# Kernel optimization log

Hardware: AMD Instinct MI355X
Metric: run time of the kernel (lower is better)

Reference implementation:

```python
import jax, jax.numpy as jnp
import numpy as np

N_ITER = 5
NMF_EPS = 1e-20
IP_EPS = 1e-20

M, J, I, K = 2, 2000, 2049, 8  # channels == sources, frames, freq bins, NMF bases


def setup_inputs() -> dict:
    key = jax.random.key(0)
    k1, k2, k3 = jax.random.split(key, 3)
    X = jax.random.normal(k1, (M, J, I, 2), dtype=jnp.float32)
    lo = 1e-08
    T0 = jax.random.uniform(k2, (I, K, M), dtype=jnp.float32) * (1 - lo) + lo
    V0 = jax.random.uniform(k3, (K, J, M), dtype=jnp.float32) * (1 - lo) + lo
    return {"X": X, "T0": T0, "V0": V0}


def nmf_update(T, V, Y, eps):
    # T: (I,K), V: (K,J), Y: (I,J) complex
    P = jnp.abs(Y) ** 2                       # power spectrogram (I,J)
    R = T @ V                                  # low-rank model (I,J)
    T = T * jnp.sqrt(((P / (R * R)) @ V.T) / ((1.0 / R) @ V.T))
    T = jnp.maximum(T, eps)
    R = T @ V
    V = V * jnp.sqrt((T.T @ (P / (R * R))) / (T.T @ (1.0 / R)))
    V = jnp.maximum(V, eps)
    R = T @ V
    return T, V, R


def reference(X, T0, V0):
    Mc, Jc, Ic, _ = X.shape
    N = Mc
    # view_as_complex(X.permute(2,0,1,3)) -> (I, M, J) complex
    Xc = jnp.transpose(X[..., 0] + 1j * X[..., 1], (2, 0, 1)).astype(jnp.complex64)
    eye_M = jnp.eye(Mc, dtype=jnp.complex64)
    W = jnp.broadcast_to(eye_M, (Ic, N, Mc))   # (I, N, M)
    T, V = T0, V0

    def body(carry, _):
        W, T, V = carry
        Y = jnp.einsum('inm,imj->inj', W, Xc)  # (I, N, J)
        for n in range(N):
            Tn, Vn, Rn = nmf_update(T[:, :, n], V[:, :, n], Y[:, n, :], NMF_EPS)
            T = T.at[:, :, n].set(Tn)
            V = V.at[:, :, n].set(Vn)
            inv_Rn = 1.0 / (Rn + IP_EPS)                       # (I, J)
            Xw = Xc * jnp.sqrt(inv_Rn)[:, None, :]             # (I, M, J)
            D = jnp.einsum('imj,ikj->imk', Xw, jnp.conj(Xw)) / Jc  # (I, M, M)
            Dreg = D + IP_EPS * eye_M
            A = jnp.einsum('inm,imk->ink', W, Dreg)            # (I, M, M)
            e_n = jnp.broadcast_to(eye_M[:, n], (Ic, Mc))
            b = jnp.linalg.solve(A, e_n[..., None])[..., 0]    # (I, M)
            quad = jnp.einsum('im,imk,ik->i', jnp.conj(b), Dreg, b)
            denom = jnp.sqrt(jnp.real(quad) + IP_EPS)          # (I,)
            W = W.at[:, n, :].set(jnp.conj(b / denom[:, None]))
        return (W, T, V), None

    (W, T, V), _ = jax.lax.scan(body, (W, T, V), None, length=N_ITER)
    Y = jnp.einsum('inm,imj->inj', W, Xc)                      # (I, N, J)
    Yp = jnp.transpose(Y, (1, 2, 0))                           # (N, J, I)
    return jnp.stack([jnp.real(Yp), jnp.imag(Yp)], axis=-1)    # (N, J, I, 2)
```

## Files before the change

### kernel.cpp

```cpp
#include <hip/hip_runtime.h>
#include <hip/hip_bf16.h>

#define M_CH 2
#define J_F 2000
#define I_F 2049
#define K_B 8
#define N_IT 5
#define NMF_EPS 1e-20f
#define IP_EPS 1e-20f
#define JCH 50
#define JCHSZ 40
#define PJT 50
#define PJSZ 40
#define IB 2304

__global__ void k_init(const float* __restrict__ T0, const float* __restrict__ V0,
                       float* __restrict__ T, float* __restrict__ V, float* __restrict__ W) {
  int t = blockIdx.x * blockDim.x + threadIdx.x;
  int stride = gridDim.x * blockDim.x;
  for (int idx = t; idx < 2 * I_F * K_B; idx += stride) {
    int n = idx / (I_F * K_B);
    int r = idx % (I_F * K_B);
    int i = r / K_B, k = r % K_B;
    T[idx] = T0[(i * K_B + k) * M_CH + n];
  }
  for (int idx = t; idx < 2 * K_B * J_F; idx += stride) {
    int n = idx / (K_B * J_F);
    int r = idx % (K_B * J_F);
    int k = r / J_F, j = r % J_F;
    V[idx] = V0[(k * J_F + j) * M_CH + n];
  }
  for (int i = t; i < I_F; i += stride) {
    W[i * 8 + 0] = 1.f; W[i * 8 + 1] = 0.f; W[i * 8 + 2] = 0.f; W[i * 8 + 3] = 0.f;
    W[i * 8 + 4] = 0.f; W[i * 8 + 5] = 0.f; W[i * 8 + 6] = 1.f; W[i * 8 + 7] = 0.f;
  }
}

__global__ __launch_bounds__(256) void k_P_T(const float2* __restrict__ X,
                                             const float* __restrict__ W,
                                             const float* __restrict__ T,
                                             const float* __restrict__ V,
                                             float* __restrict__ P,
                                             float* __restrict__ Tpart) {
  __shared__ float Vl[K_B][PJSZ];
  const int n = blockIdx.z;
  const int tid = threadIdx.x;
  const int j0 = blockIdx.y * PJSZ;
  for (int idx = tid; idx < K_B * PJSZ; idx += 256) {
    int k = idx / PJSZ, jj = idx % PJSZ;
    Vl[k][jj] = V[((size_t)n * K_B + k) * J_F + j0 + jj];
  }
  __syncthreads();
  const int i = blockIdx.x * 256 + tid;
  if (i >= I_F) return;
  float tr[K_B];
#pragma unroll
  for (int k = 0; k < K_B; ++k) tr[k] = T[((size_t)n * I_F + i) * 8 + k];
  const float4 w = ((const float4*)W)[i * 2 + n];
  float num[K_B] = {}, den[K_B] = {};
  const float2* Xa = X + i;
  const float2* Xb = X + (size_t)J_F * I_F + i;
  float* Pn = P + ((size_t)n * J_F + j0) * I_F + i;
#pragma unroll 4
  for (int jj = 0; jj < PJSZ; ++jj) {
    const size_t jo = (size_t)(j0 + jj) * I_F;
    float2 x0 = Xa[jo];
    float2 x1 = Xb[jo];
    float yr = w.x * x0.x - w.y * x0.y + w.z * x1.x - w.w * x1.y;
    float yi = w.x * x0.y + w.y * x0.x + w.z * x1.y + w.w * x1.x;
    float p = yr * yr + yi * yi;
    Pn[(size_t)jj * I_F] = p;
    float R = 0.f;
#pragma unroll
    for (int k = 0; k < K_B; ++k) R += tr[k] * Vl[k][jj];
    float a = p / (R * R);
    float b = 1.0f / R;
#pragma unroll
    for (int k = 0; k < K_B; ++k) { num[k] += a * Vl[k][jj]; den[k] += b * Vl[k][jj]; }
  }
  float* base = Tpart + (((size_t)n * PJT + blockIdx.y) * IB + i) * 16;
  *(float4*)(base + 0)  = make_float4(num[0], num[1], num[2], num[3]);
  *(float4*)(base + 4)  = make_float4(num[4], num[5], num[6], num[7]);
  *(float4*)(base + 8)  = make_float4(den[0], den[1], den[2], den[3]);
  *(float4*)(base + 12) = make_float4(den[4], den[5], den[6], den[7]);
}

__global__ __launch_bounds__(256) void k_t_finish(const float* __restrict__ Tpart,
                                                  float* __restrict__ T) {
  int t = blockIdx.x * 256 + threadIdx.x;
  if (t >= 2 * I_F * K_B) return;
  int n = t / (I_F * K_B);
  int r = t % (I_F * K_B);
  int i = r >> 3, k = r & 7;
  float num = 0.f, den = 0.f;
  const float* p = Tpart + (((size_t)n * PJT) * IB + i) * 16;
#pragma unroll 5
  for (int jt = 0; jt < PJT; ++jt) {
    num += p[(size_t)jt * IB * 16 + k];
    den += p[(size_t)jt * IB * 16 + 8 + k];
  }
  float told = T[t];
  T[t] = fmaxf(told * sqrtf(num / den), NMF_EPS);
}

__global__ __launch_bounds__(256) void k_v_update(const float* __restrict__ P,
                                                  const float* __restrict__ T,
                                                  float* __restrict__ V) {
  const int j = blockIdx.x;
  const int n = blockIdx.y;
  const int tid = threadIdx.x;
  const float* Pn = P + ((size_t)n * J_F + j) * I_F;
  const float* Tn = T + (size_t)n * I_F * K_B;
  float vold[K_B];
#pragma unroll
  for (int k = 0; k < K_B; ++k) vold[k] = V[((size_t)n * K_B + k) * J_F + j];
  float num[K_B] = {}, den[K_B] = {};
  for (int i = tid; i < I_F; i += 256) {
    float p = Pn[i];
    const float4 ta = *(const float4*)&Tn[i * 8];
    const float4 tb = *(const float4*)&Tn[i * 8 + 4];
    float tk[K_B] = {ta.x, ta.y, ta.z, ta.w, tb.x, tb.y, tb.z, tb.w};
    float R = 0.f;
#pragma unroll
    for (int k = 0; k < K_B; ++k) R += tk[k] * vold[k];
    float a = p / (R * R);
    float b = 1.0f / R;
#pragma unroll
    for (int k = 0; k < K_B; ++k) { num[k] += a * tk[k]; den[k] += b * tk[k]; }
  }
  __shared__ float red[4][16];
  const int lane = tid & 63, wid = tid >> 6;
#pragma unroll
  for (int k = 0; k < K_B; ++k) {
    float a = num[k], b = den[k];
#pragma unroll
    for (int off = 32; off > 0; off >>= 1) {
      a += __shfl_xor(a, off, 64);
      b += __shfl_xor(b, off, 64);
    }
    if (lane == 0) { red[wid][k] = a; red[wid][8 + k] = b; }
  }
  __syncthreads();
  if (tid < 16) red[0][tid] = red[0][tid] + red[1][tid] + red[2][tid] + red[3][tid];
  __syncthreads();
  if (tid < 8) {
    float vo = V[((size_t)n * K_B + tid) * J_F + j];
    V[((size_t)n * K_B + tid) * J_F + j] =
        fmaxf(vo * sqrtf(red[0][tid] / red[0][8 + tid]), NMF_EPS);
  }
}

__global__ __launch_bounds__(256) void k_d_partial(const float2* __restrict__ X,
                                                   const float* __restrict__ T,
                                                   const float* __restrict__ V,
                                                   float* __restrict__ Dpart) {
  __shared__ float Vl[K_B][JCHSZ];
  const int n = blockIdx.z;
  const int tid = threadIdx.x;
  const int j0 = blockIdx.y * JCHSZ;
  for (int idx = tid; idx < K_B * JCHSZ; idx += 256) {
    int k = idx / JCHSZ, jj = idx % JCHSZ;
    Vl[k][jj] = V[((size_t)n * K_B + k) * J_F + j0 + jj];
  }
  __syncthreads();
  const int i = blockIdx.x * 256 + tid;
  if (i >= I_F) return;
  float tr[K_B];
#pragma unroll
  for (int k = 0; k < K_B; ++k) tr[k] = T[((size_t)n * I_F + i) * K_B + k];
  float a00 = 0.f, a11 = 0.f, a01r = 0.f, a01i = 0.f;
  const float2* Xa = X + i;
  const float2* Xb = X + (size_t)J_F * I_F + i;
#pragma unroll 4
  for (int jj = 0; jj < JCHSZ; ++jj) {
    const size_t jo = (size_t)(j0 + jj) * I_F;
    float R = 0.f;
#pragma unroll
    for (int k = 0; k < K_B; ++k) R += tr[k] * Vl[k][jj];
    float wv = 1.0f / (R + IP_EPS);
    float2 x0 = Xa[jo];
    float2 x1 = Xb[jo];
    a00 += wv * (x0.x * x0.x + x0.y * x0.y);
    a11 += wv * (x1.x * x1.x + x1.y * x1.y);
    a01r += wv * (x0.x * x1.x + x0.y * x1.y);
    a01i += wv * (x0.y * x1.x - x0.x * x1.y);
  }
  ((float4*)Dpart)[((size_t)n * JCH + blockIdx.y) * I_F + i] =
      make_float4(a00, a11, a01r, a01i);
}

__global__ __launch_bounds__(256) void k_d_solve(const float* __restrict__ Dpart,
                                                 float* __restrict__ W) {
  const int i = blockIdx.x * 256 + threadIdx.x;
  if (i >= I_F) return;
  float4 wa = ((const float4*)W)[i * 2];
  float4 wb = ((const float4*)W)[i * 2 + 1];
  float w00r = wa.x, w00i = wa.y, w01r = wa.z, w01i = wa.w;
  float w10r = wb.x, w10i = wb.y, w11r = wb.z, w11i = wb.w;
  const float invJ = 1.0f / (float)J_F;
#pragma unroll
  for (int n = 0; n < 2; ++n) {
    float d00 = 0.f, d11 = 0.f, d01r = 0.f, d01i = 0.f;
    const float4* dp = (const float4*)Dpart + (size_t)n * JCH * I_F + i;
#pragma unroll 5
    for (int c = 0; c < JCH; ++c) {
      float4 d = dp[(size_t)c * I_F];
      d00 += d.x; d11 += d.y; d01r += d.z; d01i += d.w;
    }
    d00 = d00 * invJ + IP_EPS;
    d11 = d11 * invJ + IP_EPS;
    d01r *= invJ; d01i *= invJ;
    float A00r = w00r * d00 + (w01r * d01r + w01i * d01i);
    float A00i = w00i * d00 + (w01i * d01r - w01r * d01i);
    float A01r = (w00r * d01r - w00i * d01i) + w01r * d11;
    float A01i = (w00r * d01i + w00i * d01r) + w01i * d11;
    float A10r = w10r * d00 + (w11r * d01r + w11i * d01i);
    float A10i = w10i * d00 + (w11i * d01r - w11r * d01i);
    float A11r = (w10r * d01r - w10i * d01i) + w11r * d11;
    float A11i = (w10r * d01i + w10i * d01r) + w11i * d11;
    float detr = (A00r * A11r - A00i * A11i) - (A01r * A10r - A01i * A10i);
    float deti = (A00r * A11i + A00i * A11r) - (A01r * A10i + A01i * A10r);
    float idet = 1.0f / (detr * detr + deti * deti);
    float n0r, n0i, n1r, n1i;
    if (n == 0) { n0r = A11r; n0i = A11i; n1r = -A10r; n1i = -A10i; }
    else        { n0r = -A01r; n0i = -A01i; n1r = A00r; n1i = A00i; }
    float b0r = (n0r * detr + n0i * deti) * idet;
    float b0i = (n0i * detr - n0r * deti) * idet;
    float b1r = (n1r * detr + n1i * deti) * idet;
    float b1i = (n1i * detr - n1r * deti) * idet;
    float cr = d01r * b1r - d01i * b1i;
    float ci = d01r * b1i + d01i * b1r;
    float quad = d00 * (b0r * b0r + b0i * b0i) + d11 * (b1r * b1r + b1i * b1i)
               + 2.0f * (b0r * cr + b0i * ci);
    float s = 1.0f / sqrtf(quad + IP_EPS);
    if (n == 0) { w00r = b0r * s; w00i = -b0i * s; w01r = b1r * s; w01i = -b1i * s; }
    else        { w10r = b0r * s; w10i = -b0i * s; w11r = b1r * s; w11i = -b1i * s; }
  }
  ((float4*)W)[i * 2]     = make_float4(w00r, w00i, w01r, w01i);
  ((float4*)W)[i * 2 + 1] = make_float4(w10r, w10i, w11r, w11i);
}

__global__ __launch_bounds__(256) void k_final(const float2* __restrict__ X,
                                               const float* __restrict__ W,
                                               float2* __restrict__ out) {
  const int i = blockIdx.x * 256 + threadIdx.x;
  if (i >= I_F) return;
  const float4 wa = ((const float4*)W)[i * 2];
  const float4 wb = ((const float4*)W)[i * 2 + 1];
  const int j0 = blockIdx.y * 8;
  const int jend = min(8, J_F - j0);
  for (int jj = 0; jj < jend; ++jj) {
    const int j = j0 + jj;
    float2 x0 = X[(size_t)j * I_F + i];
    float2 x1 = X[(size_t)(J_F + j) * I_F + i];
    float y0r = wa.x * x0.x - wa.y * x0.y + wa.z * x1.x - wa.w * x1.y;
    float y0i = wa.x * x0.y + wa.y * x0.x + wa.z * x1.y + wa.w * x1.x;
    out[(size_t)j * I_F + i] = make_float2(y0r, y0i);
    float y1r = wb.x * x0.x - wb.y * x0.y + wb.z * x1.x - wb.w * x1.y;
    float y1i = wb.x * x0.y + wb.y * x0.x + wb.z * x1.y + wb.w * x1.x;
    out[(size_t)(J_F + j) * I_F + i] = make_float2(y1r, y1i);
  }
}

extern "C" void kernel_launch(void* const* d_in, const int* in_sizes, int n_in,
                              void* d_out, int out_size, void* d_ws, size_t ws_size,
                              hipStream_t stream) {
  const float2* X = (const float2*)d_in[0];
  const float* T0 = (const float*)d_in[1];
  const float* V0 = (const float*)d_in[2];
  char* ws = (char*)d_ws;
  size_t off = 0;
  auto alloc = [&](size_t bytes) -> void* {
    void* p = ws + off;
    off = (off + bytes + 255) & ~(size_t)255;
    return p;
  };
  float* W = (float*)alloc((size_t)I_F * 8 * 4);
  float* T = (float*)alloc((size_t)2 * I_F * K_B * 4);
  float* V = (float*)alloc((size_t)2 * K_B * J_F * 4);
  float* P = (float*)alloc((size_t)2 * I_F * J_F * 4);
  float* Scr = (float*)alloc((size_t)2 * PJT * IB * 16 * 4);
  float* Tpart = Scr;
  float* Dpart = Scr;

  k_init<<<128, 256, 0, stream>>>(T0, V0, T, V, W);
  for (int it = 0; it < N_IT; ++it) {
    k_P_T<<<dim3(9, PJT, 2), 256, 0, stream>>>(X, W, T, V, P, Tpart);
    k_t_finish<<<129, 256, 0, stream>>>(Tpart, T);
    k_v_update<<<dim3(J_F, 2), 256, 0, stream>>>(P, T, V);
    k_d_partial<<<dim3(9, JCH, 2), 256, 0, stream>>>(X, T, V, Dpart);
    k_d_solve<<<9, 256, 0, stream>>>(Dpart, W);
  }
  k_final<<<dim3(9, 250), 256, 0, stream>>>(X, W, (float2*)d_out);
}
```

Before: 507.8 us.

## Recompute power spectrogram in V update instead of storing P; halve j-chunk sizes

Drops the intermediate power-spectrogram buffer P. The T-partial kernel no longer writes it, and the V-update kernel recomputes both sources' powers directly from X and W, processing both sources in one block so each X load serves both. This removes a large global write and read of P every iteration in exchange for extra arithmetic and W loads. The j-chunk sizes for the T and D partial kernels are halved, which doubles the grid and the partial-sum traffic to gain parallelism. The reduction unrolls are adjusted to match.

```diff
diff --git a/kernel.cpp b/kernel.cpp
--- a/kernel.cpp
+++ b/kernel.cpp
@@ -8,10 +8,10 @@
 #define N_IT 5
 #define NMF_EPS 1e-20f
 #define IP_EPS 1e-20f
-#define JCH 50
-#define JCHSZ 40
-#define PJT 50
-#define PJSZ 40
+#define JCH 100
+#define JCHSZ 20
+#define PJT 100
+#define PJSZ 20
 #define IB 2304
 
 __global__ void k_init(const float* __restrict__ T0, const float* __restrict__ V0,
@@ -36,12 +36,11 @@
   }
 }
 
-__global__ __launch_bounds__(256) void k_P_T(const float2* __restrict__ X,
-                                             const float* __restrict__ W,
-                                             const float* __restrict__ T,
-                                             const float* __restrict__ V,
-                                             float* __restrict__ P,
-                                             float* __restrict__ Tpart) {
+__global__ __launch_bounds__(256) void k_T_partial(const float2* __restrict__ X,
+                                                   const float* __restrict__ W,
+                                                   const float* __restrict__ T,
+                                                   const float* __restrict__ V,
+                                                   float* __restrict__ Tpart) {
   __shared__ float Vl[K_B][PJSZ];
   const int n = blockIdx.z;
   const int tid = threadIdx.x;
@@ -60,7 +59,6 @@
   float num[K_B] = {}, den[K_B] = {};
   const float2* Xa = X + i;
   const float2* Xb = X + (size_t)J_F * I_F + i;
-  float* Pn = P + ((size_t)n * J_F + j0) * I_F + i;
 #pragma unroll 4
   for (int jj = 0; jj < PJSZ; ++jj) {
     const size_t jo = (size_t)(j0 + jj) * I_F;
@@ -69,7 +67,6 @@
     float yr = w.x * x0.x - w.y * x0.y + w.z * x1.x - w.w * x1.y;
     float yi = w.x * x0.y + w.y * x0.x + w.z * x1.y + w.w * x1.x;
     float p = yr * yr + yi * yi;
-    Pn[(size_t)jj * I_F] = p;
     float R = 0.f;
 #pragma unroll
     for (int k = 0; k < K_B; ++k) R += tr[k] * Vl[k][jj];
@@ -94,7 +91,7 @@
   int i = r >> 3, k = r & 7;
   float num = 0.f, den = 0.f;
   const float* p = Tpart + (((size_t)n * PJT) * IB + i) * 16;
-#pragma unroll 5
+#pragma unroll 10
   for (int jt = 0; jt < PJT; ++jt) {
     num += p[(size_t)jt * IB * 16 + k];
     den += p[(size_t)jt * IB * 16 + 8 + k];
@@ -103,50 +100,77 @@
   T[t] = fmaxf(told * sqrtf(num / den), NMF_EPS);
 }
 
-__global__ __launch_bounds__(256) void k_v_update(const float* __restrict__ P,
+__global__ __launch_bounds__(256) void k_v_update(const float2* __restrict__ X,
+                                                  const float* __restrict__ W,
                                                   const float* __restrict__ T,
                                                   float* __restrict__ V) {
   const int j = blockIdx.x;
-  const int n = blockIdx.y;
   const int tid = threadIdx.x;
-  const float* Pn = P + ((size_t)n * J_F + j) * I_F;
-  const float* Tn = T + (size_t)n * I_F * K_B;
-  float vold[K_B];
-#pragma unroll
-  for (int k = 0; k < K_B; ++k) vold[k] = V[((size_t)n * K_B + k) * J_F + j];
-  float num[K_B] = {}, den[K_B] = {};
+  float vold0[K_B], vold1[K_B];
+#pragma unroll
+  for (int k = 0; k < K_B; ++k) {
+    vold0[k] = V[(size_t)k * J_F + j];
+    vold1[k] = V[(size_t)(K_B + k) * J_F + j];
+  }
+  float num0[K_B] = {}, den0[K_B] = {}, num1[K_B] = {}, den1[K_B] = {};
+  const float2* Xa = X + (size_t)j * I_F;
+  const float2* Xb = X + (size_t)(J_F + j) * I_F;
+  const float* T1 = T + (size_t)I_F * K_B;
   for (int i = tid; i < I_F; i += 256) {
-    float p = Pn[i];
-    const float4 ta = *(const float4*)&Tn[i * 8];
-    const float4 tb = *(const float4*)&Tn[i * 8 + 4];
-    float tk[K_B] = {ta.x, ta.y, ta.z, ta.w, tb.x, tb.y, tb.z, tb.w};
-    float R = 0.f;
-#pragma unroll
-    for (int k = 0; k < K_B; ++k) R += tk[k] * vold[k];
-    float a = p / (R * R);
-    float b = 1.0f / R;
-#pragma unroll
-    for (int k = 0; k < K_B; ++k) { num[k] += a * tk[k]; den[k] += b * tk[k]; }
-  }
-  __shared__ float red[4][16];
+    float2 x0 = Xa[i];
+    float2 x1 = Xb[i];
+    const float4 wa = ((const float4*)W)[i * 2];
+    const float4 wb = ((const float4*)W)[i * 2 + 1];
+    float yr = wa.x * x0.x - wa.y * x0.y + wa.z * x1.x - wa.w * x1.y;
+    float yi = wa.x * x0.y + wa.y * x0.x + wa.z * x1.y + wa.w * x1.x;
+    float p0 = yr * yr + yi * yi;
+    float zr = wb.x * x0.x - wb.y * x0.y + wb.z * x1.x - wb.w * x1.y;
+    float zi = wb.x * x0.y + wb.y * x0.x + wb.z * x1.y + wb.w * x1.x;
+    float p1 = zr * zr + zi * zi;
+    const float4 ta = *(const float4*)&T[i * 8];
+    const float4 tb = *(const float4*)&T[i * 8 + 4];
+    const float4 tc = *(const float4*)&T1[i * 8];
+    const float4 td = *(const float4*)&T1[i * 8 + 4];
+    float t0[K_B] = {ta.x, ta.y, ta.z, ta.w, tb.x, tb.y, tb.z, tb.w};
+    float t1[K_B] = {tc.x, tc.y, tc.z, tc.w, td.x, td.y, td.z, td.w};
+    float R0 = 0.f, R1 = 0.f;
+#pragma unroll
+    for (int k = 0; k < K_B; ++k) { R0 += t0[k] * vold0[k]; R1 += t1[k] * vold1[k]; }
+    float a0 = p0 / (R0 * R0), b0 = 1.0f / R0;
+    float a1 = p1 / (R1 * R1), b1 = 1.0f / R1;
+#pragma unroll
+    for (int k = 0; k < K_B; ++k) {
+      num0[k] += a0 * t0[k]; den0[k] += b0 * t0[k];
+      num1[k] += a1 * t1[k]; den1[k] += b1 * t1[k];
+    }
+  }
+  __shared__ float red[4][32];
   const int lane = tid & 63, wid = tid >> 6;
 #pragma unroll
   for (int k = 0; k < K_B; ++k) {
-    float a = num[k], b = den[k];
+    float a0 = num0[k], b0 = den0[k], a1 = num1[k], b1 = den1[k];
 #pragma unroll
     for (int off = 32; off > 0; off >>= 1) {
-      a += __shfl_xor(a, off, 64);
-      b += __shfl_xor(b, off, 64);
+      a0 += __shfl_xor(a0, off, 64);
+      b0 += __shfl_xor(b0, off, 64);
+      a1 += __shfl_xor(a1, off, 64);
+      b1 += __shfl_xor(b1, off, 64);
     }
-    if (lane == 0) { red[wid][k] = a; red[wid][8 + k] = b; }
+    if (lane == 0) {
+      red[wid][k] = a0; red[wid][8 + k] = b0;
+      red[wid][16 + k] = a1; red[wid][24 + k] = b1;
+    }
   }
   __syncthreads();
-  if (tid < 16) red[0][tid] = red[0][tid] + red[1][tid] + red[2][tid] + red[3][tid];
+  if (tid < 32) red[0][tid] = red[0][tid] + red[1][tid] + red[2][tid] + red[3][tid];
   __syncthreads();
-  if (tid < 8) {
-    float vo = V[((size_t)n * K_B + tid) * J_F + j];
-    V[((size_t)n * K_B + tid) * J_F + j] =
-        fmaxf(vo * sqrtf(red[0][tid] / red[0][8 + tid]), NMF_EPS);
+  if (tid < 16) {
+    int n = tid >> 3, k = tid & 7;
+    float num = red[0][n * 16 + k];
+    float den = red[0][n * 16 + 8 + k];
+    size_t idx = ((size_t)n * K_B + k) * J_F + j;
+    float vo = V[idx];
+    V[idx] = fmaxf(vo * sqrtf(num / den), NMF_EPS);
   }
 }
 
@@ -202,7 +226,7 @@
   for (int n = 0; n < 2; ++n) {
     float d00 = 0.f, d11 = 0.f, d01r = 0.f, d01i = 0.f;
     const float4* dp = (const float4*)Dpart + (size_t)n * JCH * I_F + i;
-#pragma unroll 5
+#pragma unroll 10
     for (int c = 0; c < JCH; ++c) {
       float4 d = dp[(size_t)c * I_F];
       d00 += d.x; d11 += d.y; d01r += d.z; d01i += d.w;
@@ -278,16 +302,15 @@
   float* W = (float*)alloc((size_t)I_F * 8 * 4);
   float* T = (float*)alloc((size_t)2 * I_F * K_B * 4);
   float* V = (float*)alloc((size_t)2 * K_B * J_F * 4);
-  float* P = (float*)alloc((size_t)2 * I_F * J_F * 4);
   float* Scr = (float*)alloc((size_t)2 * PJT * IB * 16 * 4);
   float* Tpart = Scr;
   float* Dpart = Scr;
 
   k_init<<<128, 256, 0, stream>>>(T0, V0, T, V, W);
   for (int it = 0; it < N_IT; ++it) {
-    k_P_T<<<dim3(9, PJT, 2), 256, 0, stream>>>(X, W, T, V, P, Tpart);
+    k_T_partial<<<dim3(9, PJT, 2), 256, 0, stream>>>(X, W, T, V, Tpart);
     k_t_finish<<<129, 256, 0, stream>>>(Tpart, T);
-    k_v_update<<<dim3(J_F, 2), 256, 0, stream>>>(P, T, V);
+    k_v_update<<<J_F, 256, 0, stream>>>(X, W, T, V);
     k_d_partial<<<dim3(9, JCH, 2), 256, 0, stream>>>(X, T, V, Dpart);
     k_d_solve<<<9, 256, 0, stream>>>(Dpart, W);
   }
```

Result: slower. 555.2 us (+9.3%).
